# Performance work log

Hardware: AMD Instinct MI355X
Metric: run time of the kernel (lower is better)

Reference implementation:

```python
import jax, jax.numpy as jnp
import numpy as np

B, S, D, H = 2, 2048, 1024, 16
DH = D // H


def setup_inputs() -> dict:
    key = jax.random.key(0)
    ks = jax.random.split(key, 7)
    scale = 1.0 / np.sqrt(D)
    queries = jax.random.normal(ks[0], (B, S, D), dtype=jnp.float32)
    keys_ = jax.random.normal(ks[1], (B, S, D), dtype=jnp.float32)
    values = jax.random.normal(ks[2], (B, S, D), dtype=jnp.float32)
    mask = jnp.tril(jnp.ones((S, S), dtype=jnp.int32))[None, None]  # causal [1,1,S,S]
    Wq = jax.random.normal(ks[3], (D, D), dtype=jnp.float32) * scale
    Wk = jax.random.normal(ks[4], (D, D), dtype=jnp.float32) * scale
    Wv = jax.random.normal(ks[5], (D, D), dtype=jnp.float32) * scale
    Wo = jax.random.normal(ks[6], (D, D), dtype=jnp.float32) * scale
    return {"queries": queries, "keys": keys_, "values": values, "mask": mask,
            "Wq": Wq, "Wk": Wk, "Wv": Wv, "Wo": Wo}


def reference(queries, keys, values, mask, Wq, Wk, Wv, Wo):
    # linear projections (nn.Linear, no bias): x @ W.T
    def split_heads(x, W):
        return (x @ W.T).reshape(B, -1, H, DH).transpose(0, 2, 1, 3)  # [B,H,S,DH]

    q = split_heads(queries, Wq)
    k = split_heads(keys, Wk)
    v = split_heads(values, Wv)

    scores = jnp.einsum('bhqd,bhkd->bhqk', q, k) / jnp.sqrt(jnp.float32(DH))
    scores = jnp.where(mask == 0, jnp.float32(-jnp.inf), scores)
    weights = jax.nn.softmax(scores, axis=-1)  # dropout p=0.0 -> identity
    out = jnp.einsum('bhqk,bhkd->bhqd', weights, v)
    out = out.transpose(0, 2, 1, 3).reshape(B, -1, D)
    return out @ Wo.T
```

## Files before the change

kernel.cpp:

```cpp
#include <hip/hip_runtime.h>
#include <hip/hip_bf16.h>


typedef unsigned short u16;
typedef __attribute__((ext_vector_type(8))) short bf16x8;
typedef __attribute__((ext_vector_type(4))) float f32x4;
typedef __attribute__((ext_vector_type(4))) short s16x4;

#define DEVI static __device__ __forceinline__
#define SCL 0.18033688011112042f
#define LDSW 40
#define GLDS(g, l) __builtin_amdgcn_global_load_lds( \
    (const __attribute__((address_space(1))) unsigned*)(g), \
    (__attribute__((address_space(3))) unsigned*)(l), 16, 0, 0)

DEVI u16 f2bf(float f) {
  __hip_bfloat16 h = __float2bfloat16(f);
  union { __hip_bfloat16 h; u16 u; } c; c.h = h;
  return c.u;
}

DEVI bf16x8 cvt8(f32x4 a, f32x4 b) {
  bf16x8 r;
  r[0] = (short)f2bf(a[0]); r[1] = (short)f2bf(a[1]);
  r[2] = (short)f2bf(a[2]); r[3] = (short)f2bf(a[3]);
  r[4] = (short)f2bf(b[0]); r[5] = (short)f2bf(b[1]);
  r[6] = (short)f2bf(b[2]); r[7] = (short)f2bf(b[3]);
  return r;
}

template <int F32>
DEVI bf16x8 lda8(const void* base, size_t off) {
  if constexpr (!F32) {
    return *(const bf16x8*)((const u16*)base + off);
  } else {
    const float* p = (const float*)base + off;
    return cvt8(*(const f32x4*)p, *(const f32x4*)(p + 4));
  }
}

template <int F32>
DEVI void load_pair(f32x4* lo, f32x4* hi, bf16x8* bb, const void* P,
                    size_t o0, size_t o1) {
  if constexpr (F32) {
    const float* p0 = (const float*)P + o0;
    const float* p1 = (const float*)P + o1;
    lo[0] = *(const f32x4*)p0; hi[0] = *(const f32x4*)(p0 + 4);
    lo[1] = *(const f32x4*)p1; hi[1] = *(const f32x4*)(p1 + 4);
  } else {
    bb[0] = *(const bf16x8*)((const u16*)P + o0);
    bb[1] = *(const bf16x8*)((const u16*)P + o1);
  }
}

template <int F32>
DEVI void finish_pair(f32x4* lo, f32x4* hi, bf16x8* bb, u16* dst, int le0, int le1) {
  if constexpr (F32) { bb[0] = cvt8(lo[0], hi[0]); bb[1] = cvt8(lo[1], hi[1]); }
  *(bf16x8*)(dst + le0) = bb[0];
  *(bf16x8*)(dst + le1) = bb[1];
}

DEVI void vwait4() { asm volatile("s_waitcnt vmcnt(4)" ::: "memory"); }
DEVI void vwait2() { asm volatile("s_waitcnt vmcnt(2)" ::: "memory"); }
DEVI void vwait0() { asm volatile("s_waitcnt vmcnt(0)" ::: "memory"); }

template <int MODE, int O32>
DEVI void epilogue(f32x4 (&acc)[4][4], void* C, int tileM, int tileN,
                   int wr, int wc, int lr, int lg, float oscale) {
  constexpr int N = 1024;
  if constexpr (MODE == 0) {
#pragma unroll
    for (int m = 0; m < 4; ++m) {
      const int row0 = tileM + wr + m * 16 + lg * 4;
#pragma unroll
      for (int n = 0; n < 4; ++n) {
        const int col = tileN + wc + n * 16 + lr;
#pragma unroll
        for (int j = 0; j < 4; ++j) {
          if constexpr (O32)
            ((float*)C)[(size_t)(row0 + j) * N + col] = acc[m][n][j] * oscale;
          else
            ((u16*)C)[(size_t)(row0 + j) * N + col] = f2bf(acc[m][n][j] * oscale);
        }
      }
    }
  } else if constexpr (MODE == 1) {
    u16* Cv = (u16*)C;
#pragma unroll
    for (int m = 0; m < 4; ++m) {
      const int row0 = tileM + wr + m * 16 + lg * 4;
      const int bb = row0 >> 11, s0 = row0 & 2047;
#pragma unroll
      for (int n = 0; n < 4; ++n) {
        const int col = tileN + wc + n * 16 + lr;
        s16x4 pk;
#pragma unroll
        for (int j = 0; j < 4; ++j) pk[j] = (short)f2bf(acc[m][n][j]);
        *(s16x4*)(Cv + ((size_t)(col + (bb << 10)) << 11) + s0) = pk;
      }
    }
  } else {
    u16* Cv = (u16*)C;
#pragma unroll
    for (int m = 0; m < 4; ++m) {
      const int row0 = tileM + wr + m * 16 + lg * 4;
      const int bb = row0 >> 11, s0 = row0 & 2047;
#pragma unroll
      for (int n = 0; n < 4; ++n) {
        const int col = tileN + wc + n * 16 + lr;
        const size_t base = ((size_t)((bb << 4) + (col >> 6)) * 2048 + s0) * 64 + (col & 63);
#pragma unroll
        for (int j = 0; j < 4; ++j)
          Cv[base + (size_t)j * 64] = f2bf(acc[m][n][j]);
      }
    }
  }
}

template <int F32>
__global__ void __launch_bounds__(256)
cvt_w3(const void* w0, const void* w1, const void* w2,
       u16* o0, u16* o1, u16* o2) {
  const int y = blockIdx.y;
  const void* w = (y == 0) ? w0 : ((y == 1) ? w1 : w2);
  u16* o = (y == 0) ? o0 : ((y == 1) ? o1 : o2);
  const int r = blockIdx.x * 256 + threadIdx.x;
  const int p = r >> 14, t = (r >> 9) & 31, row = (r >> 2) & 127, g = r & 3;
  const int col = t * 32 + ((g ^ ((row >> 1) & 3)) << 3);
  const size_t src = ((size_t)(p * 128 + row) << 10) + col;
  *(bf16x8*)(o + (size_t)r * 8) = lda8<F32>(w, src);
}

template <int A32, int MODE, int O32>
DEVI void gemm_core(u16* sA0, u16* sA1, u16* sW0, u16* sW1,
                    const void* A, const u16* Wb, void* C,
                    int tileM, int tileN, float oscale) {
  constexpr int K = 1024;
  const int tid = threadIdx.x;
  const int lane = tid & 63;
  const int wave = tid >> 6;
  const int wr = (wave >> 1) * 64;
  const int wc = (wave & 1) * 64;
  const int lr = lane & 15, lg = lane >> 4;

  f32x4 acc[4][4] = {};

  const int e0 = tid * 8;
  const int e1 = 2048 + tid * 8;
  const int r0 = e0 >> 5, c0 = e0 & 31;
  const int r1 = e1 >> 5, c1 = e1 & 31;
  const int le0 = r0 * LDSW + c0;
  const int le1 = r1 * LDSW + c1;
  const size_t oA0 = (size_t)(tileM + r0) * K + c0;
  const size_t oA1 = (size_t)(tileM + r1) * K + c1;

  const u16* WB = Wb + ((size_t)(tileN >> 7) * 32) * 4096 + tid * 8;
  u16* dW0 = sW0 + (tid & ~63) * 8 / 64 * 512 / 8;
  dW0 = sW0 + wave * 512;
  u16* dW1 = sW1 + wave * 512;
#define STAGE_W(tt, dst) { GLDS(WB + (size_t)(tt) * 4096, dst); \
                           GLDS(WB + (size_t)(tt) * 4096 + 2048, (dst) + 2048); }

  f32x4 eLo[2], eHi[2], oLo[2], oHi[2];
  bf16x8 eB[2], oB[2];

  load_pair<A32>(eLo, eHi, eB, A, oA0, oA1);
  STAGE_W(0, dW0);
  finish_pair<A32>(eLo, eHi, eB, sA0, le0, le1);
  load_pair<A32>(oLo, oHi, oB, A, oA0 + 32, oA1 + 32);
  if constexpr (A32) vwait4(); else vwait2();
  __syncthreads();

#pragma unroll 1
  for (int it = 0; it < 16; ++it) {
    {
      const int tE = it * 2;
      STAGE_W(tE + 1, dW1);
      bf16x8 af[4], bfr[4];
#pragma unroll
      for (int m = 0; m < 4; ++m)
        af[m] = *(const bf16x8*)(sA0 + (wr + m * 16 + lr) * LDSW + lg * 8);
#pragma unroll
      for (int n = 0; n < 4; ++n) {
        const int row = wc + n * 16 + lr;
        bfr[n] = *(const bf16x8*)(sW0 + row * 32 + ((lg ^ ((row >> 1) & 3)) << 3));
      }
      if (it < 15) load_pair<A32>(eLo, eHi, eB, A, oA0 + (tE + 2) * 32, oA1 + (tE + 2) * 32);
#pragma unroll
      for (int m = 0; m < 4; ++m)
#pragma unroll
        for (int n = 0; n < 4; ++n)
          acc[m][n] = __builtin_amdgcn_mfma_f32_16x16x32_bf16(af[m], bfr[n], acc[m][n], 0, 0, 0);
      finish_pair<A32>(oLo, oHi, oB, sA1, le0, le1);
      if (it < 15) { if constexpr (A32) vwait4(); else vwait2(); } else vwait0();
      __syncthreads();
    }
    {
      const int tO = it * 2 + 1;
      if (it < 15) STAGE_W(tO + 1, dW0);
      bf16x8 af[4], bfr[4];
#pragma unroll
      for (int m = 0; m < 4; ++m)
        af[m] = *(const bf16x8*)(sA1 + (wr + m * 16 + lr) * LDSW + lg * 8);
#pragma unroll
      for (int n = 0; n < 4; ++n) {
        const int row = wc + n * 16 + lr;
        bfr[n] = *(const bf16x8*)(sW1 + row * 32 + ((lg ^ ((row >> 1) & 3)) << 3));
      }
      if (it < 15) load_pair<A32>(oLo, oHi, oB, A, oA0 + (tO + 2) * 32, oA1 + (tO + 2) * 32);
#pragma unroll
      for (int m = 0; m < 4; ++m)
#pragma unroll
        for (int n = 0; n < 4; ++n)
          acc[m][n] = __builtin_amdgcn_mfma_f32_16x16x32_bf16(af[m], bfr[n], acc[m][n], 0, 0, 0);
      if (it < 15) {
        finish_pair<A32>(eLo, eHi, eB, sA0, le0, le1);
        if constexpr (A32) vwait4(); else vwait2();
      } else {
        vwait0();
      }
      __syncthreads();
    }
  }
#undef STAGE_W
  epilogue<MODE, O32>(acc, C, tileM, tileN, wr, wc, lr, lg, oscale);
}

DEVI void tile_remap(int& tileM, int& tileN) {
  const int i = blockIdx.x + 8 * blockIdx.y;
  const int c = i & 7, s = i >> 3;
  tileM = (c * 4 + (s & 3)) * 128;
  tileN = (s >> 2) * 128;
}

template <int IN32>
__global__ void __launch_bounds__(256, 3)
gemm_qkv(const void* __restrict__ q, const u16* __restrict__ WqB, u16* __restrict__ Qp,
         const void* __restrict__ k, const u16* __restrict__ WkB, u16* __restrict__ Kh,
         const void* __restrict__ v, const u16* __restrict__ WvB, u16* __restrict__ Vt) {
  __shared__ __align__(16) u16 sA[2][128 * LDSW];
  __shared__ __align__(16) u16 sW[2][128 * 32];
  int tileM, tileN;
  tile_remap(tileM, tileN);
  if (blockIdx.z == 0)
    gemm_core<IN32, 0, 0>(sA[0], sA[1], sW[0], sW[1], q, WqB, Qp, tileM, tileN, SCL);
  else if (blockIdx.z == 1)
    gemm_core<IN32, 2, 0>(sA[0], sA[1], sW[0], sW[1], k, WkB, Kh, tileM, tileN, 1.f);
  else
    gemm_core<IN32, 1, 0>(sA[0], sA[1], sW[0], sW[1], v, WvB, Vt, tileM, tileN, 1.f);
}

template <int O32>
__global__ void __launch_bounds__(256, 3)
gemm_out(const u16* __restrict__ A, const u16* __restrict__ WoB, void* __restrict__ C) {
  __shared__ __align__(16) u16 sA[2][128 * LDSW];
  __shared__ __align__(16) u16 sW[2][128 * 32];
  int tileM, tileN;
  tile_remap(tileM, tileN);
  gemm_core<0, 0, O32>(sA[0], sA[1], sW[0], sW[1], A, WoB, C, tileM, tileN, 1.f);
}

DEVI void stage_klds(const u16* __restrict__ Kb, const u16* __restrict__ Vb,
                     u16* sKb, u16* sVb, int kt, int w, int lane) {
  const int kr = lane >> 3;
  const int kg = (lane & 7) ^ kr;
  const u16* gk = Kb + (size_t)(kt + w * 16 + kr) * 64 + kg * 8;
  const int vr = lane >> 2;
  const int vg = (lane & 3) ^ ((lane >> 3) & 3);
  const u16* gv = Vb + (size_t)(w * 32 + vr) * 2048 + kt + vg * 8;
  u16* dk = sKb + w * 1024;
  u16* dv = sVb + w * 1024;
  GLDS(gk, dk);
  GLDS(gk + 8 * 64, dk + 512);
  GLDS(gv, dv);
  GLDS(gv + (size_t)16 * 2048, dv + 512);
}

__global__ void __launch_bounds__(128, 3)
attn_kernel(const u16* Qp, const u16* __restrict__ Kh,
            const u16* __restrict__ Vt, u16* AO) {
  __shared__ __align__(16) u16 sK[3][2048];
  __shared__ __align__(16) u16 sV[3][2048];
  const int tid = threadIdx.x;
  const int lane = tid & 63;
  const int w = tid >> 6;
  const int lr = lane & 15;
  const int lg = lane >> 4;

  const int id = blockIdx.x;
  const int xcd = id & 7;
  const int slot = id >> 3;
  const int bh = xcd * 4 + (slot & 3);
  const int band = 63 - (slot >> 2);
  const int b = bh >> 4;
  const int h = bh & 15;
  const int r0 = band * 32;

  const u16* Kb = Kh + (size_t)bh * 2048 * 64;
  const u16* Vb = Vt + (size_t)bh * 64 * 2048;

  const int qrow = r0 + w * 16 + lr;
  const u16* Qw = Qp + ((size_t)(b * 2048 + qrow) << 10) + h * 64;
  const bf16x8 qf0 = *(const bf16x8*)(Qw + lg * 8);
  const bf16x8 qf1 = *(const bf16x8*)(Qw + 32 + lg * 8);

  f32x4 o[4] = {};
  float mr = -INFINITY, ls = 0.f;
  const int nt = band + 1;

  stage_klds(Kb, Vb, sK[0], sV[0], 0, w, lane);

#pragma unroll 1
  for (int t = 0; t < nt; ++t) {
    if (t + 1 < nt) {
      const int bi = (t + 1) % 3;
      stage_klds(Kb, Vb, sK[bi], sV[bi], (t + 1) * 32, w, lane);
      asm volatile("s_waitcnt vmcnt(4)" ::: "memory");
    } else {
      asm volatile("s_waitcnt vmcnt(0)" ::: "memory");
    }
    asm volatile("s_barrier" ::: "memory");
    __builtin_amdgcn_s_setprio(1);

    {
      const int bi = t % 3;
      const u16* sKb = sK[bi];
      const u16* sVb = sV[bi];
      const int sw = lr & 7;
      const bf16x8 kf0 = *(const bf16x8*)(sKb + lr * 64 + ((lg ^ sw) * 8));
      const bf16x8 kf1 = *(const bf16x8*)(sKb + lr * 64 + (((4 + lg) ^ sw) * 8));
      const bf16x8 kf2 = *(const bf16x8*)(sKb + (16 + lr) * 64 + ((lg ^ sw) * 8));
      const bf16x8 kf3 = *(const bf16x8*)(sKb + (16 + lr) * 64 + (((4 + lg) ^ sw) * 8));

      const f32x4 z = {};
      f32x4 s0 = __builtin_amdgcn_mfma_f32_16x16x32_bf16(kf0, qf0, z, 0, 0, 0);
      s0 = __builtin_amdgcn_mfma_f32_16x16x32_bf16(kf1, qf1, s0, 0, 0, 0);
      f32x4 s1 = __builtin_amdgcn_mfma_f32_16x16x32_bf16(kf2, qf0, z, 0, 0, 0);
      s1 = __builtin_amdgcn_mfma_f32_16x16x32_bf16(kf3, qf1, s1, 0, 0, 0);

      float p[8];
#pragma unroll
      for (int j = 0; j < 4; ++j) { p[j] = s0[j]; p[4 + j] = s1[j]; }
      if (t == nt - 1) {
        const int kt0 = t * 32;
#pragma unroll
        for (int j = 0; j < 4; ++j) {
          if (kt0 + lg * 4 + j > qrow)      p[j] = -INFINITY;
          if (kt0 + 16 + lg * 4 + j > qrow) p[4 + j] = -INFINITY;
        }
      }

      const float tm = fmaxf(fmaxf(fmaxf(p[0], p[1]), fmaxf(p[2], p[3])),
                             fmaxf(fmaxf(p[4], p[5]), fmaxf(p[6], p[7])));
      if (!__all(tm <= mr + 11.5f)) {
        float tr_ = fmaxf(tm, __shfl_xor(tm, 16));
        tr_ = fmaxf(tr_, __shfl_xor(tr_, 32));
        const float mn = fmaxf(mr, tr_);
        const float fac = exp2f(mr - mn);
        mr = mn;
        ls *= fac;
#pragma unroll
        for (int j = 0; j < 4; ++j) {
          const float fj = __shfl(fac, lg * 4 + j);
#pragma unroll
          for (int d = 0; d < 4; ++d) o[d][j] *= fj;
        }
      }

#pragma unroll
      for (int i = 0; i < 8; ++i) p[i] = exp2f(p[i] - mr);
      ls += ((p[0] + p[1]) + (p[2] + p[3])) + ((p[4] + p[5]) + (p[6] + p[7]));

      bf16x8 pa;
#pragma unroll
      for (int i = 0; i < 8; ++i) pa[i] = (short)f2bf(p[i]);

      const int s2 = (lr >> 1) & 3;
#pragma unroll
      for (int d = 0; d < 4; ++d) {
        const u16* vrow = sVb + (16 * d + lr) * 32;
        const s16x4 v0 = *(const s16x4*)(vrow + (((lg >> 1) ^ s2) * 8) + (lg & 1) * 4);
        const s16x4 v1 = *(const s16x4*)(vrow + ((((lg >> 1) + 2) ^ s2) * 8) + (lg & 1) * 4);
        bf16x8 vf;
        vf[0] = v0[0]; vf[1] = v0[1]; vf[2] = v0[2]; vf[3] = v0[3];
        vf[4] = v1[0]; vf[5] = v1[1]; vf[6] = v1[2]; vf[7] = v1[3];
        o[d] = __builtin_amdgcn_mfma_f32_16x16x32_bf16(pa, vf, o[d], 0, 0, 0);
      }
    }
    __builtin_amdgcn_s_setprio(0);
  }

  float lt = ls + __shfl_xor(ls, 16);
  lt += __shfl_xor(lt, 32);
  const size_t orow = (size_t)(b * 2048 + r0 + w * 16 + lg * 4);
#pragma unroll
  for (int j = 0; j < 4; ++j) {
    const float inv = 1.0f / __shfl(lt, lg * 4 + j);
#pragma unroll
    for (int d = 0; d < 4; ++d)
      AO[(orow + j) * 1024 + h * 64 + 16 * d + lr] = f2bf(o[d][j] * inv);
  }
}

static int bytes_per_elem(void* p, long long n, void* pnext) {
  if (pnext) {
    ptrdiff_t d = (char*)pnext - (char*)p;
    if (d == n * 2) return 2;
    if (d == n * 4) return 4;
  }
  size_t sz = 0;
  if (hipMemPtrGetInfo(p, &sz) == hipSuccess && sz >= (size_t)(n * 2)) {
    if (sz < (size_t)(n * 4)) return 2;
    if (sz <= (size_t)(n * 8)) return 4;
  }
  return 4;
}

extern "C" void kernel_launch(void* const* d_in, const int* in_sizes, int n_in,
                              void* d_out, int out_size, void* d_ws, size_t ws_size,
                              hipStream_t stream) {
  void* q  = d_in[0];
  void* k  = d_in[1];
  void* v  = d_in[2];
  void* wq = d_in[4];
  void* wk = d_in[5];
  void* wv = d_in[6];
  void* wo = d_in[7];

  const int in32 = bytes_per_elem(q, in_sizes[0], k) == 4;
  const int w32  = bytes_per_elem(wq, in_sizes[4], wk) == 4;
  const int o32  = bytes_per_elem(d_out, out_size, nullptr) == 4;

  const size_t SZ = (size_t)4096 * 1024;
  const size_t WZ = (size_t)1024 * 1024;
  u16* Qp = (u16*)d_ws;
  u16* Kh = Qp + SZ;
  u16* Vt = (u16*)d_out;
  u16* AO = Qp;
  u16* WqB = Vt + SZ;
  u16* WkB = WqB + WZ;
  u16* WvB = WkB + WZ;
  u16* WoB = Kh;

  if (w32) cvt_w3<1><<<dim3(512, 3), 256, 0, stream>>>(wq, wk, wv, WqB, WkB, WvB);
  else     cvt_w3<0><<<dim3(512, 3), 256, 0, stream>>>(wq, wk, wv, WqB, WkB, WvB);

  if (in32)
    gemm_qkv<1><<<dim3(8, 32, 3), 256, 0, stream>>>(q, WqB, Qp, k, WkB, Kh, v, WvB, Vt);
  else
    gemm_qkv<0><<<dim3(8, 32, 3), 256, 0, stream>>>(q, WqB, Qp, k, WkB, Kh, v, WvB, Vt);

  attn_kernel<<<dim3(2048), 128, 0, stream>>>(Qp, Kh, Vt, AO);

  if (w32) cvt_w3<1><<<dim3(512, 1), 256, 0, stream>>>(wo, wo, wo, WoB, WoB, WoB);
  else     cvt_w3<0><<<dim3(512, 1), 256, 0, stream>>>(wo, wo, wo, WoB, WoB, WoB);

  if (o32) gemm_out<1><<<dim3(8, 32), 256, 0, stream>>>(AO, WoB, d_out);
  else     gemm_out<0><<<dim3(8, 32), 256, 0, stream>>>(AO, WoB, d_out);
}
```

Baseline: 125.0 us.

## Use 64-row query bands with four waves sharing each K/V tile

The attention kernel now runs 256-thread blocks covering 64 query rows (four waves of 16 rows) instead of 128-thread blocks covering 32 rows, and the grid halves to 1024 blocks. Each staged K/V tile in LDS is reused by twice as many waves, and each wave issues half as many global-to-LDS loads per tile. This cuts K/V traffic and the staging work per query row. The cost is coarser causal load balancing, masking on the last two tiles, and higher occupancy demands from the new launch bounds.

```diff
diff --git a/kernel.cpp b/kernel.cpp
--- a/kernel.cpp
+++ b/kernel.cpp
@@ -155,8 +155,7 @@
   const size_t oA1 = (size_t)(tileM + r1) * K + c1;
 
   const u16* WB = Wb + ((size_t)(tileN >> 7) * 32) * 4096 + tid * 8;
-  u16* dW0 = sW0 + (tid & ~63) * 8 / 64 * 512 / 8;
-  dW0 = sW0 + wave * 512;
+  u16* dW0 = sW0 + wave * 512;
   u16* dW1 = sW1 + wave * 512;
 #define STAGE_W(tt, dst) { GLDS(WB + (size_t)(tt) * 4096, dst); \
                            GLDS(WB + (size_t)(tt) * 4096 + 2048, (dst) + 2048); }
@@ -260,23 +259,20 @@
   gemm_core<0, 0, O32>(sA[0], sA[1], sW[0], sW[1], A, WoB, C, tileM, tileN, 1.f);
 }
 
-DEVI void stage_klds(const u16* __restrict__ Kb, const u16* __restrict__ Vb,
-                     u16* sKb, u16* sVb, int kt, int w, int lane) {
-  const int kr = lane >> 3;
-  const int kg = (lane & 7) ^ kr;
-  const u16* gk = Kb + (size_t)(kt + w * 16 + kr) * 64 + kg * 8;
-  const int vr = lane >> 2;
-  const int vg = (lane & 3) ^ ((lane >> 3) & 3);
-  const u16* gv = Vb + (size_t)(w * 32 + vr) * 2048 + kt + vg * 8;
-  u16* dk = sKb + w * 1024;
-  u16* dv = sVb + w * 1024;
-  GLDS(gk, dk);
-  GLDS(gk + 8 * 64, dk + 512);
-  GLDS(gv, dv);
-  GLDS(gv + (size_t)16 * 2048, dv + 512);
-}
-
-__global__ void __launch_bounds__(128, 3)
+
+DEVI void stage_klds4(const u16* __restrict__ Kb, const u16* __restrict__ Vb,
+                      u16* sKb, u16* sVb, int kt, int w, int lane) {
+  const int kr = w * 8 + (lane >> 3);
+  const int kg = (lane & 7) ^ (lane >> 3);
+  const u16* gk = Kb + (size_t)(kt + kr) * 64 + kg * 8;
+  const int vr = w * 16 + (lane >> 2);
+  const int vg = (lane & 3) ^ ((vr >> 1) & 3);
+  const u16* gv = Vb + (size_t)vr * 2048 + kt + vg * 8;
+  GLDS(gk, sKb + w * 512);
+  GLDS(gv, sVb + w * 512);
+}
+
+__global__ void __launch_bounds__(256, 4)
 attn_kernel(const u16* Qp, const u16* __restrict__ Kh,
             const u16* __restrict__ Vt, u16* AO) {
   __shared__ __align__(16) u16 sK[3][2048];
@@ -291,10 +287,10 @@
   const int xcd = id & 7;
   const int slot = id >> 3;
   const int bh = xcd * 4 + (slot & 3);
-  const int band = 63 - (slot >> 2);
+  const int bd = 31 - (slot >> 2);
   const int b = bh >> 4;
   const int h = bh & 15;
-  const int r0 = band * 32;
+  const int r0 = bd * 64;
 
   const u16* Kb = Kh + (size_t)bh * 2048 * 64;
   const u16* Vb = Vt + (size_t)bh * 64 * 2048;
@@ -306,18 +302,18 @@
 
   f32x4 o[4] = {};
   float mr = -INFINITY, ls = 0.f;
-  const int nt = band + 1;
-
-  stage_klds(Kb, Vb, sK[0], sV[0], 0, w, lane);
+  const int nt = 2 * bd + 2;
+
+  stage_klds4(Kb, Vb, sK[0], sV[0], 0, w, lane);
 
 #pragma unroll 1
   for (int t = 0; t < nt; ++t) {
     if (t + 1 < nt) {
       const int bi = (t + 1) % 3;
-      stage_klds(Kb, Vb, sK[bi], sV[bi], (t + 1) * 32, w, lane);
-      asm volatile("s_waitcnt vmcnt(4)" ::: "memory");
+      stage_klds4(Kb, Vb, sK[bi], sV[bi], (t + 1) * 32, w, lane);
+      vwait2();
     } else {
-      asm volatile("s_waitcnt vmcnt(0)" ::: "memory");
+      vwait0();
     }
     asm volatile("s_barrier" ::: "memory");
     __builtin_amdgcn_s_setprio(1);
@@ -341,7 +337,7 @@
       float p[8];
 #pragma unroll
       for (int j = 0; j < 4; ++j) { p[j] = s0[j]; p[4 + j] = s1[j]; }
-      if (t == nt - 1) {
+      if (t >= nt - 2) {
         const int kt0 = t * 32;
 #pragma unroll
         for (int j = 0; j < 4; ++j) {
@@ -450,7 +446,7 @@
   else
     gemm_qkv<0><<<dim3(8, 32, 3), 256, 0, stream>>>(q, WqB, Qp, k, WkB, Kh, v, WvB, Vt);
 
-  attn_kernel<<<dim3(2048), 128, 0, stream>>>(Qp, Kh, Vt, AO);
+  attn_kernel<<<dim3(1024), 256, 0, stream>>>(Qp, Kh, Vt, AO);
 
   if (w32) cvt_w3<1><<<dim3(512, 1), 256, 0, stream>>>(wo, wo, wo, WoB, WoB, WoB);
   else     cvt_w3<0><<<dim3(512, 1), 256, 0, stream>>>(wo, wo, wo, WoB, WoB, WoB);
```

After: 115.0 us. -8.0%, faster.
